# Optimization experiments

Measured on AMD Instinct MI355X. Metric: run time of the kernel, lower is better.

The kernel has to match this reference:

```python
import jax, jax.numpy as jnp
import numpy as np

EMBED_DIM = 2048
NUM_HEAD = 32
NUM_GROUP = 8
B, S = 2, 2048


def setup_inputs() -> dict:
    key = jax.random.key(0)
    ks = jax.random.split(key, 9)
    D = EMBED_DIM // NUM_HEAD
    kv_dim = NUM_GROUP * D
    s = 0.02
    return {
        "x": jax.random.normal(ks[0], (B, S, EMBED_DIM), dtype=jnp.float32),
        "wq_w": jax.random.normal(ks[1], (EMBED_DIM, EMBED_DIM), dtype=jnp.float32) * s,
        "wq_b": jnp.zeros((EMBED_DIM,), dtype=jnp.float32),
        "wk_w": jax.random.normal(ks[2], (kv_dim, EMBED_DIM), dtype=jnp.float32) * s,
        "wk_b": jnp.zeros((kv_dim,), dtype=jnp.float32),
        "wv_w": jax.random.normal(ks[3], (kv_dim, EMBED_DIM), dtype=jnp.float32) * s,
        "wv_b": jnp.zeros((kv_dim,), dtype=jnp.float32),
        "out_w": jax.random.normal(ks[4], (EMBED_DIM, EMBED_DIM), dtype=jnp.float32) * s,
        "out_b": jnp.zeros((EMBED_DIM,), dtype=jnp.float32),
    }


def reference(x, wq_w, wq_b, wk_w, wk_b, wv_w, wv_b, out_w, out_b):
    b, s, e = x.shape
    H, G = NUM_HEAD, NUM_GROUP
    D = e // H
    r = H // G  # repeat_times
    # projections (torch Linear: x @ W.T + b)
    q = (x @ wq_w.T + wq_b).reshape(b, s, H, D)
    k = (x @ wk_w.T + wk_b).reshape(b, s, G, D)
    v = (x @ wv_w.T + wv_b).reshape(b, s, G, D)
    # faithful to torch.concat([data]*r, dim=2): TILE along head axis
    # (q-head h uses kv-head h mod G)
    k = jnp.concatenate([k] * r, axis=2)  # [b, s, H, D]
    v = jnp.concatenate([v] * r, axis=2)
    # [b, H, s_q, s_k]
    scores = jnp.einsum("bqhd,bkhd->bhqk", q, k) / (D ** 0.5)
    # faithful to F.softmax(dim=1): softmax over the HEAD axis
    attn = jax.nn.softmax(scores, axis=1)
    o = jnp.einsum("bhqk,bkhd->bqhd", attn, v).reshape(b, s, e)
    return o @ out_w.T + out_b
```

## Files before the change

kernel.cpp:

```cpp
#include <hip/hip_runtime.h>


typedef unsigned short u16;
typedef unsigned int u32;
typedef __attribute__((ext_vector_type(8))) __bf16 bf16x8;
typedef __attribute__((ext_vector_type(4))) float f32x4;
typedef __attribute__((ext_vector_type(4))) float float4_t;

#define GLD16(ldsp, gp)                                                  \
  __builtin_amdgcn_global_load_lds(                                      \
      (__attribute__((address_space(1))) void*)(void*)(gp),              \
      (__attribute__((address_space(3))) void*)(void*)(ldsp), 16, 0, 0)

static __device__ __forceinline__ u16 f2bf(float f) {
  union { float f; u32 u; } v; v.f = f;
  u32 u = v.u;
  u32 r = (u + 0x7fffu + ((u >> 16) & 1u)) >> 16;
  return (u16)r;
}

static __device__ __forceinline__ bf16x8 ld8(const u16* p) {
  return *(const bf16x8*)p;
}

__global__ void cvt_bf16(const float* __restrict__ in, u16* __restrict__ out, int n8) {
  int i = blockIdx.x * blockDim.x + threadIdx.x;
  int stride = gridDim.x * blockDim.x;
  for (; i < n8; i += stride) {
    const float4_t* p = (const float4_t*)in + (size_t)i * 2;
    float4_t a = p[0], b = p[1];
    u32 w0 = (u32)f2bf(a[0]) | ((u32)f2bf(a[1]) << 16);
    u32 w1 = (u32)f2bf(a[2]) | ((u32)f2bf(a[3]) << 16);
    u32 w2 = (u32)f2bf(b[0]) | ((u32)f2bf(b[1]) << 16);
    u32 w3 = (u32)f2bf(b[2]) | ((u32)f2bf(b[3]) << 16);
    *(uint4*)(out + (size_t)i * 8) = make_uint4(w0, w1, w2, w3);
  }
}

template <int MODE>
__global__ __launch_bounds__(256, 2)
void gemm_bt(const u16* __restrict__ A, const u16* __restrict__ Bw,
             const float* __restrict__ bias,
             u16* __restrict__ Cb, float* __restrict__ Cf, int N) {
  constexpr int K = 2048;
  constexpr int SHSZ = (MODE == 2) ? (128 * 136) : 8192;
  __shared__ u16 sh[SHSZ];
  u16* As = sh;
  u16* Bs = sh + 4096;
  const int tid = threadIdx.x;
  const int lane = tid & 63;
  const int w = tid >> 6;
  const int m0 = blockIdx.y * 128;
  const int n0 = blockIdx.x * 128;
  const int wr = (w >> 1) * 64, wc = (w & 1) * 64;
  const int r15 = lane & 15, kq = lane >> 4;

  f32x4 acc[4][4] = {};

  for (int k0 = 0; k0 < K; k0 += 32) {
#pragma unroll
    for (int i = 0; i < 2; ++i) {
      int c = i * 256 + tid;
      int r = c >> 2, ch = c & 3;
      int sc = (ch ^ (r & 3)) * 8;
      GLD16(&As[c * 8], &A[(size_t)(m0 + r) * K + k0 + sc]);
      GLD16(&Bs[c * 8], &Bw[(size_t)(n0 + r) * K + k0 + sc]);
    }
    __syncthreads();
    bf16x8 af[4], bfr[4];
#pragma unroll
    for (int mt = 0; mt < 4; ++mt) {
      int r = wr + mt * 16 + r15;
      af[mt] = ld8(&As[r * 32 + ((kq ^ (r15 & 3)) * 8)]);
    }
#pragma unroll
    for (int nt = 0; nt < 4; ++nt) {
      int r = wc + nt * 16 + r15;
      bfr[nt] = ld8(&Bs[r * 32 + ((kq ^ (r15 & 3)) * 8)]);
    }
#pragma unroll
    for (int mt = 0; mt < 4; ++mt)
#pragma unroll
      for (int nt = 0; nt < 4; ++nt)
        acc[mt][nt] = __builtin_amdgcn_mfma_f32_16x16x32_bf16(af[mt], bfr[nt], acc[mt][nt], 0, 0, 0);
    __syncthreads();
  }

  if constexpr (MODE == 2) {
#pragma unroll
    for (int mt = 0; mt < 4; ++mt)
#pragma unroll
      for (int nt = 0; nt < 4; ++nt) {
        int col = wc + nt * 16 + r15;
        float bv = bias[n0 + col];
#pragma unroll
        for (int r = 0; r < 4; ++r) {
          int row = wr + mt * 16 + kq * 4 + r;
          sh[col * 136 + row] = f2bf(acc[mt][nt][r] + bv);
        }
      }
    __syncthreads();
    const int m0l = m0 & 2047;
    const int bb = m0 >> 11;
#pragma unroll
    for (int i = 0; i < 8; ++i) {
      int c = i * 256 + tid;
      int cc = c >> 4, so = c & 15;
      *(uint4*)&Cb[(size_t)(bb * 512 + n0 + cc) * 2048 + m0l + so * 8] =
          *(const uint4*)&sh[cc * 136 + so * 8];
    }
  } else {
    const int rb = kq * 4;
#pragma unroll
    for (int mt = 0; mt < 4; ++mt) {
#pragma unroll
      for (int nt = 0; nt < 4; ++nt) {
        int col = n0 + wc + nt * 16 + r15;
        float bv = bias[col];
#pragma unroll
        for (int r = 0; r < 4; ++r) {
          int row = m0 + wr + mt * 16 + rb + r;
          float v = acc[mt][nt][r] + bv;
          if constexpr (MODE == 0) Cb[(size_t)row * N + col] = f2bf(v);
          else                     Cf[(size_t)row * N + col] = v;
        }
      }
    }
  }
}

__global__ __launch_bounds__(1024, 4)
void attn_fused(const u16* __restrict__ Q, const u16* __restrict__ Kg,
                const u16* __restrict__ Vt, u16* __restrict__ O) {
  __shared__ float slab[8 * 528];
  __shared__ float rsb[528];
  __shared__ u16 Pl[8 * 2592];

  const int tid = threadIdx.x;
  const int lane = tid & 63, w = tid >> 6;
  const int g = w & 7, zz = w >> 3;
  const int l15 = lane & 15, kq = lane >> 4;

  const int xcd = blockIdx.x & 7;
  const int b = xcd >> 2;
  const int q0 = (((blockIdx.x >> 3) << 2) + (xcd & 3)) << 4;

  const u16* Qb = Q + (size_t)b * 2048 * 2048;
  const u16* Kb = Kg + (size_t)b * 2048 * 512;
  const u16* Vb = Vt + (size_t)b * 512 * 2048;

  bf16x8 qf[4][2];
#pragma unroll
  for (int qq = 0; qq < 4; ++qq)
#pragma unroll
    for (int t = 0; t < 2; ++t)
      qf[qq][t] = ld8(&Qb[(size_t)(q0 + qq * 4 + (l15 & 3)) * 2048 +
                          (g + 8 * (l15 >> 2)) * 64 + t * 32 + kq * 8]);

  f32x4 acc[2][2][2] = {};

  for (int k0 = 0; k0 < 2048; k0 += 32) {
    const u16* krow = &Kb[(size_t)(k0 + zz * 16 + l15) * 512 + g * 64 + kq * 8];
    bf16x8 bk0 = ld8(krow);
    bf16x8 bk1 = ld8(krow + 32);
    u32 epk[4][2];
    f32x4 su[4];
#pragma unroll
    for (int qq = 0; qq < 4; ++qq) {
      f32x4 s = {};
      s = __builtin_amdgcn_mfma_f32_16x16x32_bf16(qf[qq][0], bk0, s, 0, 0, 0);
      s = __builtin_amdgcn_mfma_f32_16x16x32_bf16(qf[qq][1], bk1, s, 0, 0, 0);
      float e0 = __expf(s[0] * 0.125f);
      float e1 = __expf(s[1] * 0.125f);
      float e2 = __expf(s[2] * 0.125f);
      float e3 = __expf(s[3] * 0.125f);
      epk[qq][0] = __builtin_amdgcn_perm(__float_as_uint(e1), __float_as_uint(e0), 0x07060302u);
      epk[qq][1] = __builtin_amdgcn_perm(__float_as_uint(e3), __float_as_uint(e2), 0x07060302u);
      f32x4 t = {e0, e1, e2, e3};
#pragma unroll
      for (int c = 0; c < 4; ++c) {
        t[c] += __shfl_xor(t[c], 16);
        t[c] += __shfl_xor(t[c], 32);
      }
      su[qq] = t;
    }
#pragma unroll
    for (int r = 0; r < 4; ++r) {
      float v = kq == 0 ? su[0][r] : kq == 1 ? su[1][r] : kq == 2 ? su[2][r] : su[3][r];
      slab[g * 528 + (kq * 4 + r) * 33 + zz * 16 + l15] = v;
    }
    __syncthreads();

    if (tid < 512) {
      int q = tid >> 5, k = tid & 31;
      float s = 0.f;
#pragma unroll
      for (int gg = 0; gg < 8; ++gg) s += slab[gg * 528 + q * 33 + k];
      rsb[q * 33 + k] = __builtin_amdgcn_rcpf(s);
    }
    __syncthreads();

#pragma unroll
    for (int qq = 0; qq < 4; ++qq) {
      float rsv[4];
#pragma unroll
      for (int r = 0; r < 4; ++r) rsv[r] = rsb[(qq * 4 + r) * 33 + zz * 16 + l15];
      u32 lo = epk[qq][0], hi = epk[qq][1];
      float p0 = __uint_as_float(lo << 16) * rsv[0];
      float p1 = __uint_as_float(lo & 0xffff0000u) * rsv[1];
      float p2 = __uint_as_float(hi << 16) * rsv[2];
      float p3 = __uint_as_float(hi & 0xffff0000u) * rsv[3];
      int base = g * 2592 + (kq >> 1) * 1296 + (qq >> 1) * 648 +
                 ((kq & 1) * 8 + (qq & 1) * 4) * 40 + zz * 16 + l15;
      Pl[base + 0 * 40] = f2bf(p0);
      Pl[base + 1 * 40] = f2bf(p1);
      Pl[base + 2 * 40] = f2bf(p2);
      Pl[base + 3 * 40] = f2bf(p3);
    }
    __syncthreads();

    bf16x8 vb[2];
#pragma unroll
    for (int nl = 0; nl < 2; ++nl)
      vb[nl] = ld8(&Vb[(size_t)(g * 64 + (zz * 2 + nl) * 16 + l15) * 2048 + k0 + kq * 8]);
#pragma unroll
    for (int pp = 0; pp < 2; ++pp)
#pragma unroll
      for (int qh = 0; qh < 2; ++qh) {
        bf16x8 pa = ld8(&Pl[g * 2592 + pp * 1296 + qh * 648 + l15 * 40 + kq * 8]);
#pragma unroll
        for (int nl = 0; nl < 2; ++nl)
          acc[pp][qh][nl] =
              __builtin_amdgcn_mfma_f32_16x16x32_bf16(pa, vb[nl], acc[pp][qh][nl], 0, 0, 0);
      }
  }

#pragma unroll
  for (int pp = 0; pp < 2; ++pp)
#pragma unroll
    for (int qh = 0; qh < 2; ++qh)
#pragma unroll
      for (int nl = 0; nl < 2; ++nl)
#pragma unroll
        for (int r = 0; r < 4; ++r) {
          int q = q0 + qh * 8 + (kq & 1) * 4 + r;
          int h = g + 8 * (2 * pp + (kq >> 1));
          O[((size_t)(b * 2048 + q)) * 2048 + h * 64 + (zz * 2 + nl) * 16 + l15] =
              f2bf(acc[pp][qh][nl][r]);
        }
}

extern "C" void kernel_launch(void* const* d_in, const int* in_sizes, int n_in,
                              void* d_out, int out_size, void* d_ws, size_t ws_size,
                              hipStream_t stream) {
  (void)in_sizes; (void)n_in; (void)out_size; (void)ws_size;
  const float* x    = (const float*)d_in[0];
  const float* wq_w = (const float*)d_in[1];
  const float* wq_b = (const float*)d_in[2];
  const float* wk_w = (const float*)d_in[3];
  const float* wk_b = (const float*)d_in[4];
  const float* wv_w = (const float*)d_in[5];
  const float* wv_b = (const float*)d_in[6];
  const float* wo_w = (const float*)d_in[7];
  const float* wo_b = (const float*)d_in[8];
  float* out = (float*)d_out;

  char* p = (char*)d_ws;
  u16* xb  = (u16*)p; p += (size_t)4096 * 2048 * 2;
  u16* wqb = (u16*)p; p += (size_t)2048 * 2048 * 2;
  u16* wkb = (u16*)p; p += (size_t)512 * 2048 * 2;
  u16* wvb = (u16*)p; p += (size_t)512 * 2048 * 2;
  u16* wob = (u16*)p; p += (size_t)2048 * 2048 * 2;
  u16* Qb  = (u16*)p; p += (size_t)4096 * 2048 * 2;
  u16* Kb  = (u16*)p; p += (size_t)4096 * 512 * 2;
  u16* Vtb = (u16*)p; p += (size_t)1024 * 2048 * 2;
  u16* Ob  = (u16*)p; p += (size_t)4096 * 2048 * 2;

  auto cvt = [&](const float* in, u16* o, int n) {
    int n8 = n / 8;
    int grid = (n8 + 255) / 256; if (grid > 2048) grid = 2048;
    hipLaunchKernelGGL(cvt_bf16, dim3(grid), dim3(256), 0, stream, in, o, n8);
  };
  cvt(x, xb, 4096 * 2048);
  cvt(wq_w, wqb, 2048 * 2048);
  cvt(wk_w, wkb, 512 * 2048);
  cvt(wv_w, wvb, 512 * 2048);
  cvt(wo_w, wob, 2048 * 2048);

  hipLaunchKernelGGL((gemm_bt<0>), dim3(16, 32), dim3(256), 0, stream,
                     xb, wqb, wq_b, Qb, (float*)nullptr, 2048);
  hipLaunchKernelGGL((gemm_bt<0>), dim3(4, 32),  dim3(256), 0, stream,
                     xb, wkb, wk_b, Kb, (float*)nullptr, 512);
  hipLaunchKernelGGL((gemm_bt<2>), dim3(4, 32),  dim3(256), 0, stream,
                     xb, wvb, wv_b, Vtb, (float*)nullptr, 512);

  hipLaunchKernelGGL(attn_fused, dim3(256), dim3(1024), 0, stream, Qb, Kb, Vtb, Ob);

  hipLaunchKernelGGL((gemm_bt<1>), dim3(16, 32), dim3(256), 0, stream,
                     Ob, wob, wo_b, (u16*)nullptr, out, 2048);
}
```

Before: 462.1 us.

## Restructure attention so P stays in registers, dropping the P LDS round-trip

```diff
diff --git a/kernel.cpp b/kernel.cpp
--- a/kernel.cpp
+++ b/kernel.cpp
@@ -21,6 +21,14 @@
 
 static __device__ __forceinline__ bf16x8 ld8(const u16* p) {
   return *(const bf16x8*)p;
+}
+
+static __device__ __forceinline__ float hsum4(float v) {
+  v += __builtin_bit_cast(float, __builtin_amdgcn_update_dpp(
+           0, __builtin_bit_cast(int, v), 0x124, 0xf, 0xf, true));
+  v += __builtin_bit_cast(float, __builtin_amdgcn_update_dpp(
+           0, __builtin_bit_cast(int, v), 0x128, 0xf, 0xf, true));
+  return v;
 }
 
 __global__ void cvt_bf16(const float* __restrict__ in, u16* __restrict__ out, int n8) {
@@ -106,8 +114,17 @@
     for (int i = 0; i < 8; ++i) {
       int c = i * 256 + tid;
       int cc = c >> 4, so = c & 15;
+      int X = cc * 136 + (so >> 2) * 32 + (so & 3) * 4;
+      u32 A0 = *(const u32*)&sh[X + 0];
+      u32 A1 = *(const u32*)&sh[X + 2];
+      u32 B0 = *(const u32*)&sh[X + 16];
+      u32 B1 = *(const u32*)&sh[X + 18];
+      u32 w0 = __builtin_amdgcn_perm(B0, A0, 0x05040100u);
+      u32 w1 = __builtin_amdgcn_perm(B0, A0, 0x07060302u);
+      u32 w2 = __builtin_amdgcn_perm(B1, A1, 0x05040100u);
+      u32 w3 = __builtin_amdgcn_perm(B1, A1, 0x07060302u);
       *(uint4*)&Cb[(size_t)(bb * 512 + n0 + cc) * 2048 + m0l + so * 8] =
-          *(const uint4*)&sh[cc * 136 + so * 8];
+          make_uint4(w0, w1, w2, w3);
     }
   } else {
     const int rb = kq * 4;
@@ -133,62 +150,72 @@
 void attn_fused(const u16* __restrict__ Q, const u16* __restrict__ Kg,
                 const u16* __restrict__ Vt, u16* __restrict__ O) {
   __shared__ float slab[8 * 528];
-  __shared__ float rsb[528];
-  __shared__ u16 Pl[8 * 2592];
+  __shared__ float rsb[16 * 36];
 
   const int tid = threadIdx.x;
   const int lane = tid & 63, w = tid >> 6;
-  const int g = w & 7, zz = w >> 3;
+  const int g = w & 7, zd = w >> 3;
   const int l15 = lane & 15, kq = lane >> 4;
+  const int qr = l15 & 3, hl = l15 >> 2;
 
   const int xcd = blockIdx.x & 7;
   const int b = xcd >> 2;
-  const int q0 = (((blockIdx.x >> 3) << 2) + (xcd & 3)) << 4;
+  const int q0 = ((((blockIdx.x >> 3) << 2) + (xcd & 3)) << 4);
+  const int qbase = q0 + zd * 8;
 
   const u16* Qb = Q + (size_t)b * 2048 * 2048;
   const u16* Kb = Kg + (size_t)b * 2048 * 512;
   const u16* Vb = Vt + (size_t)b * 512 * 2048;
 
-  bf16x8 qf[4][2];
-#pragma unroll
-  for (int qq = 0; qq < 4; ++qq)
+  bf16x8 qf[2][2];
+#pragma unroll
+  for (int qq = 0; qq < 2; ++qq)
 #pragma unroll
     for (int t = 0; t < 2; ++t)
-      qf[qq][t] = ld8(&Qb[(size_t)(q0 + qq * 4 + (l15 & 3)) * 2048 +
-                          (g + 8 * (l15 >> 2)) * 64 + t * 32 + kq * 8]);
-
-  f32x4 acc[2][2][2] = {};
+      qf[qq][t] = ld8(&Qb[(size_t)(qbase + qq * 4 + qr) * 2048 +
+                          (g + 8 * hl) * 64 + t * 32 + kq * 8]);
+
+  f32x4 acc[2][4] = {};
 
   for (int k0 = 0; k0 < 2048; k0 += 32) {
-    const u16* krow = &Kb[(size_t)(k0 + zz * 16 + l15) * 512 + g * 64 + kq * 8];
-    bf16x8 bk0 = ld8(krow);
-    bf16x8 bk1 = ld8(krow + 32);
-    u32 epk[4][2];
-    f32x4 su[4];
-#pragma unroll
-    for (int qq = 0; qq < 4; ++qq) {
-      f32x4 s = {};
-      s = __builtin_amdgcn_mfma_f32_16x16x32_bf16(qf[qq][0], bk0, s, 0, 0, 0);
-      s = __builtin_amdgcn_mfma_f32_16x16x32_bf16(qf[qq][1], bk1, s, 0, 0, 0);
-      float e0 = __expf(s[0] * 0.125f);
-      float e1 = __expf(s[1] * 0.125f);
-      float e2 = __expf(s[2] * 0.125f);
-      float e3 = __expf(s[3] * 0.125f);
-      epk[qq][0] = __builtin_amdgcn_perm(__float_as_uint(e1), __float_as_uint(e0), 0x07060302u);
-      epk[qq][1] = __builtin_amdgcn_perm(__float_as_uint(e3), __float_as_uint(e2), 0x07060302u);
-      f32x4 t = {e0, e1, e2, e3};
-#pragma unroll
-      for (int c = 0; c < 4; ++c) {
-        t[c] += __shfl_xor(t[c], 16);
-        t[c] += __shfl_xor(t[c], 32);
+    bf16x8 kf[2][2];
+#pragma unroll
+    for (int ko = 0; ko < 2; ++ko)
+#pragma unroll
+      for (int t = 0; t < 2; ++t)
+        kf[ko][t] = ld8(&Kb[(size_t)(k0 + ko * 16 + l15) * 512 +
+                            g * 64 + t * 32 + kq * 8]);
+
+    f32x4 sc[2][2];
+#pragma unroll
+    for (int qq = 0; qq < 2; ++qq)
+#pragma unroll
+      for (int ko = 0; ko < 2; ++ko) {
+        f32x4 s = {};
+        s = __builtin_amdgcn_mfma_f32_16x16x32_bf16(kf[ko][0], qf[qq][0], s, 0, 0, 0);
+        s = __builtin_amdgcn_mfma_f32_16x16x32_bf16(kf[ko][1], qf[qq][1], s, 0, 0, 0);
+#pragma unroll
+        for (int r = 0; r < 4; ++r) s[r] = exp2f(s[r] * 0.18033688f);
+        sc[qq][ko] = s;
       }
-      su[qq] = t;
-    }
-#pragma unroll
-    for (int r = 0; r < 4; ++r) {
-      float v = kq == 0 ? su[0][r] : kq == 1 ? su[1][r] : kq == 2 ? su[2][r] : su[3][r];
-      slab[g * 528 + (kq * 4 + r) * 33 + zz * 16 + l15] = v;
-    }
+
+#pragma unroll
+    for (int qq = 0; qq < 2; ++qq)
+#pragma unroll
+      for (int ko = 0; ko < 2; ++ko) {
+#pragma unroll
+        for (int r = 0; r < 4; ++r) {
+          float su = hsum4(sc[qq][ko][r]);
+          if (hl == 0)
+            slab[g * 528 + (zd * 8 + qq * 4 + qr) * 33 + ko * 16 + kq * 4 + r] = su;
+        }
+      }
+
+    bf16x8 vb[4];
+#pragma unroll
+    for (int nt = 0; nt < 4; ++nt)
+      vb[nt] = ld8(&Vb[(size_t)(g * 64 + nt * 16 + l15) * 2048 + k0 + kq * 8]);
+
     __syncthreads();
 
     if (tid < 512) {
@@ -196,58 +223,35 @@
       float s = 0.f;
 #pragma unroll
       for (int gg = 0; gg < 8; ++gg) s += slab[gg * 528 + q * 33 + k];
-      rsb[q * 33 + k] = __builtin_amdgcn_rcpf(s);
-    }
-    __syncthreads();
-
-#pragma unroll
-    for (int qq = 0; qq < 4; ++qq) {
-      float rsv[4];
-#pragma unroll
-      for (int r = 0; r < 4; ++r) rsv[r] = rsb[(qq * 4 + r) * 33 + zz * 16 + l15];
-      u32 lo = epk[qq][0], hi = epk[qq][1];
-      float p0 = __uint_as_float(lo << 16) * rsv[0];
-      float p1 = __uint_as_float(lo & 0xffff0000u) * rsv[1];
-      float p2 = __uint_as_float(hi << 16) * rsv[2];
-      float p3 = __uint_as_float(hi & 0xffff0000u) * rsv[3];
-      int base = g * 2592 + (kq >> 1) * 1296 + (qq >> 1) * 648 +
-                 ((kq & 1) * 8 + (qq & 1) * 4) * 40 + zz * 16 + l15;
-      Pl[base + 0 * 40] = f2bf(p0);
-      Pl[base + 1 * 40] = f2bf(p1);
-      Pl[base + 2 * 40] = f2bf(p2);
-      Pl[base + 3 * 40] = f2bf(p3);
-    }
-    __syncthreads();
-
-    bf16x8 vb[2];
-#pragma unroll
-    for (int nl = 0; nl < 2; ++nl)
-      vb[nl] = ld8(&Vb[(size_t)(g * 64 + (zz * 2 + nl) * 16 + l15) * 2048 + k0 + kq * 8]);
-#pragma unroll
-    for (int pp = 0; pp < 2; ++pp)
-#pragma unroll
-      for (int qh = 0; qh < 2; ++qh) {
-        bf16x8 pa = ld8(&Pl[g * 2592 + pp * 1296 + qh * 648 + l15 * 40 + kq * 8]);
-#pragma unroll
-        for (int nl = 0; nl < 2; ++nl)
-          acc[pp][qh][nl] =
-              __builtin_amdgcn_mfma_f32_16x16x32_bf16(pa, vb[nl], acc[pp][qh][nl], 0, 0, 0);
-      }
+      rsb[q * 36 + k] = __builtin_amdgcn_rcpf(s);
+    }
+    __syncthreads();
+
+#pragma unroll
+    for (int qq = 0; qq < 2; ++qq) {
+      const int ql = zd * 8 + qq * 4 + qr;
+      f32x4 rs0 = *(const f32x4*)&rsb[ql * 36 + 0 * 16 + kq * 4];
+      f32x4 rs1 = *(const f32x4*)&rsb[ql * 36 + 1 * 16 + kq * 4];
+      u32 paw[4];
+#pragma unroll
+      for (int r = 0; r < 4; ++r)
+        paw[r] = (u32)f2bf(sc[qq][0][r] * rs0[r]) |
+                 ((u32)f2bf(sc[qq][1][r] * rs1[r]) << 16);
+      bf16x8 pa = __builtin_bit_cast(bf16x8, *(uint4*)paw);
+#pragma unroll
+      for (int nt = 0; nt < 4; ++nt)
+        acc[qq][nt] = __builtin_amdgcn_mfma_f32_16x16x32_bf16(pa, vb[nt], acc[qq][nt], 0, 0, 0);
+    }
   }
 
 #pragma unroll
-  for (int pp = 0; pp < 2; ++pp)
-#pragma unroll
-    for (int qh = 0; qh < 2; ++qh)
-#pragma unroll
-      for (int nl = 0; nl < 2; ++nl)
-#pragma unroll
-        for (int r = 0; r < 4; ++r) {
-          int q = q0 + qh * 8 + (kq & 1) * 4 + r;
-          int h = g + 8 * (2 * pp + (kq >> 1));
-          O[((size_t)(b * 2048 + q)) * 2048 + h * 64 + (zz * 2 + nl) * 16 + l15] =
-              f2bf(acc[pp][qh][nl][r]);
-        }
+  for (int qq = 0; qq < 2; ++qq)
+#pragma unroll
+    for (int nt = 0; nt < 4; ++nt)
+#pragma unroll
+      for (int r = 0; r < 4; ++r)
+        O[(size_t)(b * 2048 + qbase + qq * 4 + r) * 2048 +
+          (g + 8 * kq) * 64 + nt * 16 + l15] = f2bf(acc[qq][nt][r]);
 }
 
 extern "C" void kernel_launch(void* const* d_in, const int* in_sizes, int n_in,
```

Result: faster. 448.0 us (-3.0%).
